# Optimization experiments

Hardware: AMD Instinct MI355X
Metric: run time of the kernel (lower is better)

The kernel has to match this reference:

```python
import jax, jax.numpy as jnp
import numpy as np
import math

EMBED_DIM = 1024
NUM_HEADS = 16
HEAD_DIM = EMBED_DIM // NUM_HEADS
D_FF = 4 * EMBED_DIM
EPS = 1e-6  # flax LayerNorm default


def _layer_norm(x, scale, bias):
    mu = jnp.mean(x, axis=-1, keepdims=True)
    var = jnp.mean(jnp.square(x - mu), axis=-1, keepdims=True)
    return (x - mu) * jax.lax.rsqrt(var + EPS) * scale + bias


def setup_inputs() -> dict:
    key = jax.random.key(0)
    ks = jax.random.split(key, 12)
    B, T, D = 8, 1024, EMBED_DIM
    x = jax.random.normal(ks[0], (B, T, D), dtype=jnp.float32)
    # causal mask broadcastable to [B, H, T, T]
    mask = jnp.tril(jnp.ones((T, T), dtype=bool))[None, None, :, :]
    mask = jnp.broadcast_to(mask, (B, 1, T, T))
    s = 0.02
    return {
        "x": x,
        "mask": mask,
        "ln1_scale": jnp.ones((D,), jnp.float32),
        "ln1_bias": jnp.zeros((D,), jnp.float32),
        "wq": jax.random.normal(ks[1], (D, D), jnp.float32) * s,
        "bq": jnp.zeros((D,), jnp.float32),
        "wk": jax.random.normal(ks[2], (D, D), jnp.float32) * s,
        "bk": jnp.zeros((D,), jnp.float32),
        "wv": jax.random.normal(ks[3], (D, D), jnp.float32) * s,
        "bv": jnp.zeros((D,), jnp.float32),
        "wo": jax.random.normal(ks[4], (D, D), jnp.float32) * s,
        "bo": jnp.zeros((D,), jnp.float32),
        "ln2_scale": jnp.ones((D,), jnp.float32),
        "ln2_bias": jnp.zeros((D,), jnp.float32),
        "w1": jax.random.normal(ks[5], (D, D_FF), jnp.float32) * s,
        "b1": jnp.zeros((D_FF,), jnp.float32),
        "w2": jax.random.normal(ks[6], (D_FF, D), jnp.float32) * s,
        "b2": jnp.zeros((D,), jnp.float32),
    }


def reference(x, mask, ln1_scale, ln1_bias, wq, bq, wk, bk, wv, bv, wo, bo,
              ln2_scale, ln2_bias, w1, b1, w2, b2):
    B, T, D = x.shape
    residual = x
    h = _layer_norm(x, ln1_scale, ln1_bias)
    q = (h @ wq + bq).reshape(B, T, NUM_HEADS, HEAD_DIM)
    k = (h @ wk + bk).reshape(B, T, NUM_HEADS, HEAD_DIM)
    v = (h @ wv + bv).reshape(B, T, NUM_HEADS, HEAD_DIM)
    # scores: [B, H, T, T]
    scores = jnp.einsum("bqhd,bkhd->bhqk", q, k) / math.sqrt(HEAD_DIM)
    scores = jnp.where(mask, scores, -1e9)
    probs = jax.nn.softmax(scores, axis=-1)
    # dropout is identity (deterministic=True)
    out = jnp.einsum("bhqk,bkhd->bqhd", probs, v).reshape(B, T, D)
    h = out @ wo + bo
    x = h + residual
    residual = x
    h = _layer_norm(x, ln2_scale, ln2_bias)
    h = jax.nn.gelu(h @ w1 + b1, approximate=True)  # flax nn.gelu default
    h = h @ w2 + b2
    return h + residual
```

## Files before the change

kernel.cpp:

```cpp
#include <hip/hip_runtime.h>
#include <hip/hip_bf16.h>

using bf16 = __hip_bfloat16;
typedef __attribute__((ext_vector_type(8))) short bf16x8;
typedef __attribute__((ext_vector_type(4))) float f32x4;

__device__ inline float u2f(unsigned int u) { return __uint_as_float(u << 16); }
__device__ inline float toF(float x) { return x; }
__device__ inline float toF(bf16 x) { return __bfloat162float(x); }
__device__ inline void storeO(float* p, float v) { *p = v; }
__device__ inline void storeO(bf16* p, float v) { *p = __float2bfloat16(v); }

__device__ inline void gload_lds16(const void* g, void* l) {
    __builtin_amdgcn_global_load_lds(
        (const __attribute__((address_space(1))) void*)g,
        (__attribute__((address_space(3))) void*)l, 16, 0, 0);
}

__device__ inline int swzb(int row, int bcol) {
    return row * 128 + (bcol ^ (((row ^ (row >> 3)) & 7) << 4));
}

__global__ __launch_bounds__(256) void transpose_k(const float* __restrict__ in,
                                                   bf16* __restrict__ out,
                                                   int R, int C) {
    __shared__ float tile[32][33];
    const int c0 = blockIdx.x * 32, r0 = blockIdx.y * 32;
    const int tx = threadIdx.x & 31, ty = threadIdx.x >> 5;
#pragma unroll
    for (int i = 0; i < 32; i += 8)
        tile[ty + i][tx] = in[(size_t)(r0 + ty + i) * C + (c0 + tx)];
    __syncthreads();
#pragma unroll
    for (int i = 0; i < 32; i += 8)
        out[(size_t)(c0 + ty + i) * R + (r0 + tx)] = __float2bfloat16(tile[tx][ty + i]);
}

__global__ __launch_bounds__(256) void catb_k(const float* __restrict__ a,
                                              const float* __restrict__ b,
                                              const float* __restrict__ c,
                                              float* __restrict__ o) {
    const int t = blockIdx.x * 256 + threadIdx.x;
    const float* s = t < 1024 ? a : (t < 2048 ? b : c);
    o[t] = s[t & 1023];
}

__device__ inline float waveRedSum(float x) {
#pragma unroll
    for (int off = 32; off; off >>= 1) x += __shfl_xor(x, off, 64);
    return x;
}

template <typename T>
__global__ __launch_bounds__(256) void layernorm_k(const T* __restrict__ in,
                                                   const float* __restrict__ g,
                                                   const float* __restrict__ bta,
                                                   bf16* __restrict__ out) {
    const int row = blockIdx.x, t = threadIdx.x;
    const int lane = t & 63, wid = t >> 6;
    const T* xr = in + (size_t)row * 1024;
    float v0, v1, v2, v3;
    if constexpr (sizeof(T) == 4) {
        float4 u = ((const float4*)xr)[t];
        v0 = u.x; v1 = u.y; v2 = u.z; v3 = u.w;
    } else {
        ushort4 u = ((const ushort4*)xr)[t];
        v0 = u2f(u.x); v1 = u2f(u.y); v2 = u2f(u.z); v3 = u2f(u.w);
    }
    __shared__ float red[8];
    float s = waveRedSum(v0 + v1 + v2 + v3);
    if (lane == 0) red[wid] = s;
    __syncthreads();
    float mu = (red[0] + red[1] + red[2] + red[3]) * (1.f / 1024.f);
    float d0 = v0 - mu, d1 = v1 - mu, d2 = v2 - mu, d3 = v3 - mu;
    float ss = waveRedSum(d0 * d0 + d1 * d1 + d2 * d2 + d3 * d3);
    if (lane == 0) red[4 + wid] = ss;
    __syncthreads();
    float var = (red[4] + red[5] + red[6] + red[7]) * (1.f / 1024.f);
    float inv = rsqrtf(var + 1e-6f);
    const int c = t * 4;
    bf16* orow = out + (size_t)row * 1024;
    orow[c + 0] = __float2bfloat16(d0 * inv * g[c + 0] + bta[c + 0]);
    orow[c + 1] = __float2bfloat16(d1 * inv * g[c + 1] + bta[c + 1]);
    orow[c + 2] = __float2bfloat16(d2 * inv * g[c + 2] + bta[c + 2]);
    orow[c + 3] = __float2bfloat16(d3 * inv * g[c + 3] + bta[c + 3]);
}

template <int GELU, int RES, int ACC, typename RT, typename OT>
__global__ __launch_bounds__(256) void mgemm_k(const bf16* __restrict__ A,
                                               const bf16* __restrict__ B, int ldB,
                                               const float* __restrict__ bias,
                                               const RT* __restrict__ resid,
                                               OT* C, int M, int N, int K) {
    __shared__ bf16 As[128 * 32];
    __shared__ bf16 Bs[128 * 32];
    const int tid = threadIdx.x;
    const int lane = tid & 63, wid = tid >> 6;
    const int l16 = lane & 15, quad = lane >> 4;
    const int wm = (wid >> 1) * 64, wn = (wid & 1) * 64;
    const int m0 = blockIdx.y * 128, n0 = blockIdx.x * 128;

    const int r0 = tid >> 2, sc0 = tid & 3;
    const int lc0 = sc0 ^ ((r0 >> 1) & 3);
    const int r1 = r0 + 64;
    const int lc1 = sc0 ^ ((r1 >> 1) & 3);
    const bf16* gA0 = A + (size_t)(m0 + r0) * K + lc0 * 8;
    const bf16* gA1 = A + (size_t)(m0 + r1) * K + lc1 * 8;
    const bf16* gB0 = B + (size_t)(n0 + r0) * ldB + lc0 * 8;
    const bf16* gB1 = B + (size_t)(n0 + r1) * ldB + lc1 * 8;
    char* asb = (char*)As;
    char* bsb = (char*)Bs;
    const int lb0 = wid * 1024, lb1 = 4096 + wid * 1024;
    const int rdsw = (quad ^ ((l16 >> 1) & 3)) * 16;

    f32x4 acc[4][4] = {};
    for (int k0 = 0; k0 < K; k0 += 32) {
        __syncthreads();
        gload_lds16(gA0 + k0, asb + lb0);
        gload_lds16(gA1 + k0, asb + lb1);
        gload_lds16(gB0 + k0, bsb + lb0);
        gload_lds16(gB1 + k0, bsb + lb1);
        __syncthreads();
        bf16x8 a[4], b[4];
#pragma unroll
        for (int i = 0; i < 4; ++i)
            a[i] = *(const bf16x8*)(asb + (wm + i * 16 + l16) * 64 + rdsw);
#pragma unroll
        for (int i = 0; i < 4; ++i)
            b[i] = *(const bf16x8*)(bsb + (wn + i * 16 + l16) * 64 + rdsw);
#pragma unroll
        for (int mi = 0; mi < 4; ++mi)
#pragma unroll
            for (int ni = 0; ni < 4; ++ni)
                acc[mi][ni] = __builtin_amdgcn_mfma_f32_16x16x32_bf16(
                    a[mi], b[ni], acc[mi][ni], 0, 0, 0);
    }
#pragma unroll
    for (int mi = 0; mi < 4; ++mi) {
#pragma unroll
        for (int ni = 0; ni < 4; ++ni) {
            const int col = n0 + wn + ni * 16 + l16;
            const float bv = bias ? bias[col] : 0.f;
#pragma unroll
            for (int r = 0; r < 4; ++r) {
                const int row = m0 + wm + mi * 16 + quad * 4 + r;
                float val = acc[mi][ni][r] + bv;
                if (GELU) {
                    float z = 0.7978845608028654f * (val + 0.044715f * val * val * val);
                    float th = 1.f - 2.f / (__expf(2.f * z) + 1.f);
                    val = 0.5f * val * (1.f + th);
                }
                const size_t idx = (size_t)row * N + col;
                if (RES) val += toF(resid[idx]);
                if (ACC) val += toF(C[idx]);
                storeO(&C[idx], val);
            }
        }
    }
}

__global__ __launch_bounds__(256) void attn_k(const bf16* __restrict__ q,
                                              const bf16* __restrict__ k,
                                              const bf16* __restrict__ v,
                                              bf16* __restrict__ o, int rs) {
    const int b = blockIdx.z, h = blockIdx.y;
    const int qblock = blockIdx.x * 256;
    const int tid = threadIdx.x;
    const int wave = tid >> 6, lane = tid & 63;
    const int l16 = lane & 15, quad = lane >> 4;
    const int q0w = qblock + wave * 64;

    __shared__ __align__(16) bf16 Kl[64 * 64];
    __shared__ __align__(16) bf16 Vt[64 * 64];
    __shared__ __align__(16) bf16 Pl[4 * 64 * 64];
    __shared__ __align__(16) float sc[4][64];

    bf16x8 qf[4][2];
#pragma unroll
    for (int ni = 0; ni < 4; ++ni) {
        const int row = q0w + ni * 16 + l16;
        const bf16* qp = q + ((size_t)b * 1024 + row) * rs + h * 64;
#pragma unroll
        for (int kc = 0; kc < 2; ++kc)
            qf[ni][kc] = *(const bf16x8*)(qp + kc * 32 + quad * 8);
    }

    f32x4 acc[4][4] = {};
    float mrun[4], lrun[4];
#pragma unroll
    for (int ni = 0; ni < 4; ++ni) { mrun[ni] = -1e30f; lrun[ni] = 0.f; }

    const int NT = blockIdx.x * 4 + 4;
    const int myNT = blockIdx.x * 4 + wave + 1;
    for (int t = 0; t < NT; ++t) {
        const int j0 = t * 64;
        __syncthreads();
        {
            const int r = tid >> 3, ch = tid & 7;
#pragma unroll
            for (int p = 0; p < 2; ++p) {
                const int row = r + p * 32;
                const size_t g = ((size_t)b * 1024 + j0 + row) * rs + h * 64 + ch * 8;
                *(uint4*)((char*)Kl + swzb(row, ch * 16)) = *(const uint4*)(k + g);
            }
        }
        {
            const int r = (tid >> 3) * 2;
            const int dbase = (tid & 7) * 8;
            const size_t g0 = ((size_t)b * 1024 + j0 + r) * rs + h * 64 + dbase;
            const uint4 A4 = *(const uint4*)(v + g0);
            const uint4 B4 = *(const uint4*)(v + g0 + rs);
            const unsigned aw[4] = {A4.x, A4.y, A4.z, A4.w};
            const unsigned bw[4] = {B4.x, B4.y, B4.z, B4.w};
#pragma unroll
            for (int j = 0; j < 8; ++j) {
                const unsigned lo = (aw[j >> 1] >> ((j & 1) * 16)) & 0xffffu;
                const unsigned hi = (bw[j >> 1] >> ((j & 1) * 16)) & 0xffffu;
                *(unsigned*)((char*)Vt + swzb(dbase + j, r * 2)) = lo | (hi << 16);
            }
        }
        __syncthreads();
        if (t < myNT) {
            f32x4 st[4][4] = {};
#pragma unroll
            for (int kc = 0; kc < 2; ++kc) {
                bf16x8 kf[4];
#pragma unroll
                for (int mi = 0; mi < 4; ++mi)
                    kf[mi] = *(const bf16x8*)((char*)Kl +
                             swzb(mi * 16 + l16, kc * 64 + quad * 16));
#pragma unroll
                for (int mi = 0; mi < 4; ++mi)
#pragma unroll
                    for (int ni = 0; ni < 4; ++ni)
                        st[mi][ni] = __builtin_amdgcn_mfma_f32_16x16x32_bf16(
                            kf[mi], qf[ni][kc], st[mi][ni], 0, 0, 0);
            }
            if (j0 == q0w) {
#pragma unroll
                for (int mi = 0; mi < 4; ++mi)
#pragma unroll
                    for (int ni = 0; ni < 4; ++ni)
#pragma unroll
                        for (int r = 0; r < 4; ++r)
                            if (mi * 16 + quad * 4 + r > ni * 16 + l16)
                                st[mi][ni][r] = -1e30f;
            }
            float fac[4];
#pragma unroll
            for (int ni = 0; ni < 4; ++ni) {
                float mx = -1e30f;
#pragma unroll
                for (int mi = 0; mi < 4; ++mi)
#pragma unroll
                    for (int r = 0; r < 4; ++r) mx = fmaxf(mx, st[mi][ni][r]);
                mx = fmaxf(mx, __shfl_xor(mx, 16, 64));
                mx = fmaxf(mx, __shfl_xor(mx, 32, 64));
                const float nm = fmaxf(mrun[ni], mx);
                fac[ni] = __expf((mrun[ni] - nm) * 0.125f);
                mrun[ni] = nm;
                float ls = 0.f;
#pragma unroll
                for (int mi = 0; mi < 4; ++mi)
#pragma unroll
                    for (int r = 0; r < 4; ++r) {
                        const float p = __expf((st[mi][ni][r] - nm) * 0.125f);
                        st[mi][ni][r] = p;
                        ls += p;
                    }
                ls += __shfl_xor(ls, 16, 64);
                ls += __shfl_xor(ls, 32, 64);
                lrun[ni] = lrun[ni] * fac[ni] + ls;
            }
            if (quad == 0)
#pragma unroll
                for (int ni = 0; ni < 4; ++ni) sc[wave][ni * 16 + l16] = fac[ni];
#pragma unroll
            for (int mi = 0; mi < 4; ++mi) {
                const f32x4 f4 = *(const f32x4*)&sc[wave][mi * 16 + quad * 4];
#pragma unroll
                for (int ni = 0; ni < 4; ++ni)
#pragma unroll
                    for (int r = 0; r < 4; ++r) acc[mi][ni][r] *= f4[r];
            }
            char* Pb = (char*)Pl + wave * 8192;
#pragma unroll
            for (int ni = 0; ni < 4; ++ni) {
                const int qrow = ni * 16 + l16;
#pragma unroll
                for (int mi = 0; mi < 4; ++mi) {
                    union { bf16 bv[4]; uint2 u2; } pk;
#pragma unroll
                    for (int r = 0; r < 4; ++r)
                        pk.bv[r] = __float2bfloat16(st[mi][ni][r]);
                    *(uint2*)(Pb + swzb(qrow, mi * 32 + quad * 8)) = pk.u2;
                }
            }
#pragma unroll
            for (int kc = 0; kc < 2; ++kc) {
                bf16x8 pf[4], vf[4];
#pragma unroll
                for (int mi = 0; mi < 4; ++mi)
                    pf[mi] = *(const bf16x8*)(Pb +
                             swzb(mi * 16 + l16, kc * 64 + quad * 16));
#pragma unroll
                for (int ni = 0; ni < 4; ++ni)
                    vf[ni] = *(const bf16x8*)((char*)Vt +
                             swzb(ni * 16 + l16, kc * 64 + quad * 16));
#pragma unroll
                for (int mi = 0; mi < 4; ++mi)
#pragma unroll
                    for (int ni = 0; ni < 4; ++ni)
                        acc[mi][ni] = __builtin_amdgcn_mfma_f32_16x16x32_bf16(
                            pf[mi], vf[ni], acc[mi][ni], 0, 0, 0);
            }
        }
    }
    if (quad == 0)
#pragma unroll
        for (int ni = 0; ni < 4; ++ni) sc[wave][ni * 16 + l16] = lrun[ni];
#pragma unroll
    for (int mi = 0; mi < 4; ++mi) {
        const f32x4 l4 = *(const f32x4*)&sc[wave][mi * 16 + quad * 4];
#pragma unroll
        for (int r = 0; r < 4; ++r) {
            const float inv = 1.f / l4[r];
            const int row = q0w + mi * 16 + quad * 4 + r;
            bf16* orow = o + ((size_t)b * 1024 + row) * 1024 + h * 64;
#pragma unroll
            for (int ni = 0; ni < 4; ++ni)
                orow[ni * 16 + l16] = __float2bfloat16(acc[mi][ni][r] * inv);
        }
    }
}

extern "C" void kernel_launch(void* const* d_in, const int* in_sizes, int n_in,
                              void* d_out, int out_size, void* d_ws, size_t ws_size,
                              hipStream_t stream) {
    (void)out_size; (void)ws_size;
    const float* x = (const float*)d_in[0];
    const int base = (n_in >= 18 && in_sizes[1] > 4096) ? 2 : 1;
    const float* ln1s = (const float*)d_in[base + 0];
    const float* ln1b = (const float*)d_in[base + 1];
    const float* wq   = (const float*)d_in[base + 2];
    const float* bq   = (const float*)d_in[base + 3];
    const float* wk   = (const float*)d_in[base + 4];
    const float* bk   = (const float*)d_in[base + 5];
    const float* wv   = (const float*)d_in[base + 6];
    const float* bv   = (const float*)d_in[base + 7];
    const float* wo   = (const float*)d_in[base + 8];
    const float* bo   = (const float*)d_in[base + 9];
    const float* ln2s = (const float*)d_in[base + 10];
    const float* ln2b = (const float*)d_in[base + 11];
    const float* w1   = (const float*)d_in[base + 12];
    const float* b1   = (const float*)d_in[base + 13];
    const float* w2   = (const float*)d_in[base + 14];
    const float* b2   = (const float*)d_in[base + 15];
    float* out = (float*)d_out;

    char* ws = (char*)d_ws;
    char* oc = (char*)d_out;
    const size_t MB = 1ull << 20;
    bf16* h     = (bf16*)(ws + 0 * MB);
    bf16* qkv   = (bf16*)(ws + 16 * MB);
    bf16* ao    = (bf16*)(ws + 0 * MB);
    bf16* h2    = (bf16*)(ws + 0 * MB);
    bf16* woT   = (bf16*)(ws + 16 * MB);
    bf16* f1c   = (bf16*)(ws + 16 * MB);
    bf16* w1T   = (bf16*)(ws + 48 * MB);
    bf16* w2T   = (bf16*)(ws + 56 * MB);
    bf16* wqkvT = (bf16*)(oc + 0 * MB);
    float* bqkv = (float*)(oc + 8 * MB);

    const dim3 tb(256);

    layernorm_k<float><<<8192, tb, 0, stream>>>(x, ln1s, ln1b, h);
    transpose_k<<<dim3(32, 32), tb, 0, stream>>>(wq, wqkvT, 1024, 1024);
    transpose_k<<<dim3(32, 32), tb, 0, stream>>>(wk, wqkvT + 1024 * 1024, 1024, 1024);
    transpose_k<<<dim3(32, 32), tb, 0, stream>>>(wv, wqkvT + 2 * 1024 * 1024, 1024, 1024);
    catb_k<<<12, tb, 0, stream>>>(bq, bk, bv, bqkv);
    mgemm_k<0, 0, 0, float, bf16><<<dim3(24, 64), tb, 0, stream>>>(
        h, wqkvT, 1024, bqkv, nullptr, qkv, 8192, 3072, 1024);
    attn_k<<<dim3(4, 16, 8), tb, 0, stream>>>(qkv, qkv + 1024, qkv + 2048, ao, 3072);
    transpose_k<<<dim3(32, 32), tb, 0, stream>>>(wo, woT, 1024, 1024);
    transpose_k<<<dim3(128, 32), tb, 0, stream>>>(w1, w1T, 1024, 4096);
    transpose_k<<<dim3(32, 128), tb, 0, stream>>>(w2, w2T, 4096, 1024);
    mgemm_k<0, 1, 0, float, float><<<dim3(8, 64), tb, 0, stream>>>(
        ao, woT, 1024, bo, x, out, 8192, 1024, 1024);
    layernorm_k<float><<<8192, tb, 0, stream>>>(out, ln2s, ln2b, h2);
    for (int c = 0; c < 2; ++c) {
        mgemm_k<1, 0, 0, float, bf16><<<dim3(16, 64), tb, 0, stream>>>(
            h2, w1T + (size_t)c * 2048 * 1024, 1024, b1 + c * 2048, nullptr,
            f1c, 8192, 2048, 1024);
        mgemm_k<0, 0, 1, float, float><<<dim3(8, 64), tb, 0, stream>>>(
            f1c, w2T + c * 2048, 4096, c ? nullptr : b2, nullptr,
            out, 8192, 1024, 2048);
    }
}
```

Before: 698.5 us.

## Double-buffer GEMM LDS tiles and prefetch attention K/V into registers

```diff
diff --git a/kernel.cpp b/kernel.cpp
--- a/kernel.cpp
+++ b/kernel.cpp
@@ -15,6 +15,12 @@
     __builtin_amdgcn_global_load_lds(
         (const __attribute__((address_space(1))) void*)g,
         (__attribute__((address_space(3))) void*)l, 16, 0, 0);
+}
+
+__device__ inline void wgbar() {
+    asm volatile("s_waitcnt lgkmcnt(0)" ::: "memory");
+    __builtin_amdgcn_s_barrier();
+    asm volatile("" ::: "memory");
 }
 
 __device__ inline int swzb(int row, int bcol) {
@@ -92,8 +98,8 @@
                                                const float* __restrict__ bias,
                                                const RT* __restrict__ resid,
                                                OT* C, int M, int N, int K) {
-    __shared__ bf16 As[128 * 32];
-    __shared__ bf16 Bs[128 * 32];
+    __shared__ bf16 As[2 * 128 * 32];
+    __shared__ bf16 Bs[2 * 128 * 32];
     const int tid = threadIdx.x;
     const int lane = tid & 63, wid = tid >> 6;
     const int l16 = lane & 15, quad = lane >> 4;
@@ -114,26 +120,39 @@
     const int rdsw = (quad ^ ((l16 >> 1) & 3)) * 16;
 
     f32x4 acc[4][4] = {};
-    for (int k0 = 0; k0 < K; k0 += 32) {
-        __syncthreads();
-        gload_lds16(gA0 + k0, asb + lb0);
-        gload_lds16(gA1 + k0, asb + lb1);
-        gload_lds16(gB0 + k0, bsb + lb0);
-        gload_lds16(gB1 + k0, bsb + lb1);
-        __syncthreads();
+    const int nT = K >> 5;
+    gload_lds16(gA0, asb + lb0);
+    gload_lds16(gA1, asb + lb1);
+    gload_lds16(gB0, bsb + lb0);
+    gload_lds16(gB1, bsb + lb1);
+    __syncthreads();
+    for (int t = 0; t < nT; ++t) {
+        const int cur = t & 1;
+        if (t + 1 < nT) {
+            char* ab = asb + (cur ^ 1) * 8192;
+            char* bb = bsb + (cur ^ 1) * 8192;
+            const int ko = (t + 1) * 32;
+            gload_lds16(gA0 + ko, ab + lb0);
+            gload_lds16(gA1 + ko, ab + lb1);
+            gload_lds16(gB0 + ko, bb + lb0);
+            gload_lds16(gB1 + ko, bb + lb1);
+        }
+        const char* ar = asb + cur * 8192;
+        const char* br = bsb + cur * 8192;
         bf16x8 a[4], b[4];
 #pragma unroll
         for (int i = 0; i < 4; ++i)
-            a[i] = *(const bf16x8*)(asb + (wm + i * 16 + l16) * 64 + rdsw);
+            a[i] = *(const bf16x8*)(ar + (wm + i * 16 + l16) * 64 + rdsw);
 #pragma unroll
         for (int i = 0; i < 4; ++i)
-            b[i] = *(const bf16x8*)(bsb + (wn + i * 16 + l16) * 64 + rdsw);
+            b[i] = *(const bf16x8*)(br + (wn + i * 16 + l16) * 64 + rdsw);
 #pragma unroll
         for (int mi = 0; mi < 4; ++mi)
 #pragma unroll
             for (int ni = 0; ni < 4; ++ni)
                 acc[mi][ni] = __builtin_amdgcn_mfma_f32_16x16x32_bf16(
                     a[mi], b[ni], acc[mi][ni], 0, 0, 0);
+        __syncthreads();
     }
 #pragma unroll
     for (int mi = 0; mi < 4; ++mi) {
@@ -164,7 +183,8 @@
                                               const bf16* __restrict__ v,
                                               bf16* __restrict__ o, int rs) {
     const int b = blockIdx.z, h = blockIdx.y;
-    const int qblock = blockIdx.x * 256;
+    const int qi = 3 - blockIdx.x;
+    const int qblock = qi * 256;
     const int tid = threadIdx.x;
     const int wave = tid >> 6, lane = tid & 63;
     const int l16 = lane & 15, quad = lane >> 4;
@@ -190,37 +210,47 @@
 #pragma unroll
     for (int ni = 0; ni < 4; ++ni) { mrun[ni] = -1e30f; lrun[ni] = 0.f; }
 
-    const int NT = blockIdx.x * 4 + 4;
-    const int myNT = blockIdx.x * 4 + wave + 1;
+    const int NT = qi * 4 + 4;
+    const int myNT = qi * 4 + wave + 1;
+
+    const int kr_ = tid >> 3, kch = tid & 7;
+    const int vr_ = (tid >> 3) * 2, vdb = (tid & 7) * 8;
+    uint4 kA, kB, vA, vB;
+    {
+        const size_t gk = ((size_t)b * 1024 + 0 + kr_) * rs + h * 64 + kch * 8;
+        kA = *(const uint4*)(k + gk);
+        kB = *(const uint4*)(k + gk + (size_t)32 * rs);
+        const size_t gv = ((size_t)b * 1024 + 0 + vr_) * rs + h * 64 + vdb;
+        vA = *(const uint4*)(v + gv);
+        vB = *(const uint4*)(v + gv + rs);
+    }
+
     for (int t = 0; t < NT; ++t) {
-        const int j0 = t * 64;
-        __syncthreads();
+        wgbar();
+        *(uint4*)((char*)Kl + swzb(kr_, kch * 16)) = kA;
+        *(uint4*)((char*)Kl + swzb(kr_ + 32, kch * 16)) = kB;
         {
-            const int r = tid >> 3, ch = tid & 7;
-#pragma unroll
-            for (int p = 0; p < 2; ++p) {
-                const int row = r + p * 32;
-                const size_t g = ((size_t)b * 1024 + j0 + row) * rs + h * 64 + ch * 8;
-                *(uint4*)((char*)Kl + swzb(row, ch * 16)) = *(const uint4*)(k + g);
-            }
-        }
-        {
-            const int r = (tid >> 3) * 2;
-            const int dbase = (tid & 7) * 8;
-            const size_t g0 = ((size_t)b * 1024 + j0 + r) * rs + h * 64 + dbase;
-            const uint4 A4 = *(const uint4*)(v + g0);
-            const uint4 B4 = *(const uint4*)(v + g0 + rs);
-            const unsigned aw[4] = {A4.x, A4.y, A4.z, A4.w};
-            const unsigned bw[4] = {B4.x, B4.y, B4.z, B4.w};
+            const unsigned aw[4] = {vA.x, vA.y, vA.z, vA.w};
+            const unsigned bw[4] = {vB.x, vB.y, vB.z, vB.w};
 #pragma unroll
             for (int j = 0; j < 8; ++j) {
                 const unsigned lo = (aw[j >> 1] >> ((j & 1) * 16)) & 0xffffu;
                 const unsigned hi = (bw[j >> 1] >> ((j & 1) * 16)) & 0xffffu;
-                *(unsigned*)((char*)Vt + swzb(dbase + j, r * 2)) = lo | (hi << 16);
-            }
-        }
-        __syncthreads();
+                *(unsigned*)((char*)Vt + swzb(vdb + j, vr_ * 2)) = lo | (hi << 16);
+            }
+        }
+        if (t + 1 < NT) {
+            const int j1 = (t + 1) * 64;
+            const size_t gk = ((size_t)b * 1024 + j1 + kr_) * rs + h * 64 + kch * 8;
+            kA = *(const uint4*)(k + gk);
+            kB = *(const uint4*)(k + gk + (size_t)32 * rs);
+            const size_t gv = ((size_t)b * 1024 + j1 + vr_) * rs + h * 64 + vdb;
+            vA = *(const uint4*)(v + gv);
+            vB = *(const uint4*)(v + gv + rs);
+        }
+        wgbar();
         if (t < myNT) {
+            const int j0 = t * 64;
             f32x4 st[4][4] = {};
 #pragma unroll
             for (int kc = 0; kc < 2; ++kc) {
```

New measurement: 642.0 us. -8.1%, faster.
